# Optimization experiments

Measured on AMD Instinct MI355X. Metric: run time of the kernel, lower is better.

Reference implementation:

```python
import jax, jax.numpy as jnp
import numpy as np

NU = 8192   # num_users
NI = 8192   # num_items
B = 4096    # batch_size
D = 64      # embed_size
NS = 5      # num_scores


def _w(key, fan_in, fan_out):
    # xavier-uniform-like init
    lim = np.sqrt(6.0 / (fan_in + fan_out)).astype(np.float32)
    return jax.random.uniform(key, (fan_in, fan_out), jnp.float32, -lim, lim)


def setup_inputs() -> dict:
    key = jax.random.key(0)
    ks = jax.random.split(key, 32)
    z = lambda n: jnp.zeros((n,), jnp.float32)
    inp = {
        "batch_user": jax.random.randint(ks[0], (B,), 0, NU),
        "batch_item": jax.random.randint(ks[1], (B,), 0, NI),
        "R": jax.random.uniform(ks[2], (NU, NI), jnp.float32),
        "S": jax.random.uniform(ks[3], (NU, NU), jnp.float32),
        "U": _w(ks[4], NU, D),
        "V": _w(ks[5], NI, D),
        "w_r": _w(ks[6], NS, D), "b_r": z(D),
        "Wu0": _w(ks[7], 2 * D, D), "bu0": z(D), "Wu1": _w(ks[8], D, D), "bu1": z(D),
        "Wv0": _w(ks[9], 2 * D, D), "bv0": z(D), "Wv1": _w(ks[10], D, D), "bv1": z(D),
        "Wc0": _w(ks[11], 2 * D, D), "bc0": z(D), "Wc1": _w(ks[12], D, D), "bc1": z(D),
        "Wg0": _w(ks[13], 2 * D, D), "bg0": z(D), "Wg1": _w(ks[14], D, D), "bg1": z(D),
        "W_I": _w(ks[15], D, D), "b_I": z(D),
        "W_Sm": _w(ks[16], D, D), "b_Sm": z(D),
        "W1A": _w(ks[17], 2 * D, D), "b1A": z(D), "w2A": _w(ks[18], D, 1), "b2A": z(1),
        "W1B": _w(ks[19], 2 * D, D), "b1B": z(D), "w2B": _w(ks[20], D, 1), "b2B": z(1),
        "W1M": _w(ks[21], 2 * D, D), "b1M": z(D), "w2M": _w(ks[22], D, 1), "b2M": z(1),
        "W_Z": _w(ks[23], D, D), "b_Z": z(D),
    }
    return inp


def reference(batch_user, batch_item, R, S, U, V, w_r, b_r,
              Wu0, bu0, Wu1, bu1, Wv0, bv0, Wv1, bv1,
              Wc0, bc0, Wc1, bc1, Wg0, bg0, Wg1, bg1,
              W_I, b_I, W_Sm, b_Sm,
              W1A, b1A, w2A, b2A, W1B, b1B, w2B, b2B,
              W1M, b1M, w2M, b2M, W_Z, b_Z):
    relu = jax.nn.relu
    # rating embedding: e_r = Linear(num_scores->d) applied to vector [1..num_scores]
    e_r = jnp.arange(1, w_r.shape[0] + 1, dtype=w_r.dtype) @ w_r + b_r  # [d]
    Uc = jnp.concatenate([U, jnp.broadcast_to(e_r, U.shape)], axis=1)  # [NU, 2d]
    Vc = jnp.concatenate([V, jnp.broadcast_to(e_r, V.shape)], axis=1)  # [NI, 2d]
    # per-node MLP stacks (num_layer=2; layer0: 2d->d, layer1: d->d)
    Uh = relu(relu(Uc @ Wu0 + bu0) @ Wu1 + bu1)  # [NU, d]
    Vh = relu(relu(Vc @ Wv0 + bv0) @ Wv1 + bv1)  # [NI, d]
    Ub = Uh[batch_user]  # [B, d]
    Vb = Vh[batch_item]  # [B, d]
    # item-space attention A over batch, softmax along batch dim
    A = jax.nn.softmax(relu(jnp.concatenate([Vb, Ub], axis=1) @ W1A + b1A) @ w2A + b2A, axis=0)  # [B,1]
    # attention-weighted sparse-row aggregation over item embeddings
    H_I = relu(((R[batch_user] * A) @ Vh) @ W_I + b_I)  # [B, d]
    Bw = jax.nn.softmax(relu(jnp.concatenate([H_I, Ub], axis=1) @ W1B + b1B) @ w2B + b2B, axis=0)  # [B,1]
    H_S = relu(((S[batch_user] * Bw) @ Uh) @ W_Sm + b_Sm)  # [B, d]
    H = jnp.concatenate([H_I, H_S], axis=1)  # [B, 2d]
    H = relu(relu(H @ Wc0 + bc0) @ Wc1 + bc1)  # [B, d]
    M = jax.nn.softmax(relu(jnp.concatenate([Ub, Vb], axis=1) @ W1M + b1M) @ w2M + b2M, axis=0)  # [B,1]
    # R.T row-gather: columns of R for batch items -> [B, NU]
    Rt_b = jnp.take(R, batch_item, axis=1).T
    Z = relu(((Rt_b * M) @ Uh) @ W_Z + b_Z)  # [B, d]
    G = jnp.concatenate([H, Z], axis=1)  # [B, 2d]
    G = relu(relu(G @ Wg0 + bg0) @ Wg1 + bg1)  # [B, d]
    return G
```

## Files before the change

### kernel.cpp

```cpp
#include <hip/hip_runtime.h>
#include <stdint.h>


typedef short bf16x8 __attribute__((ext_vector_type(8)));
typedef float f32x4 __attribute__((ext_vector_type(4)));

__device__ __forceinline__ unsigned f2bf1(float f) {
    unsigned x = __float_as_uint(f);
    return (x + 0x7FFFu + ((x >> 16) & 1u)) >> 16;
}

__device__ __forceinline__ float wsum(float v) {
    #pragma unroll
    for (int o = 32; o; o >>= 1) v += __shfl_xor(v, o);
    return v;
}

__device__ __forceinline__ void block_softmax_stats(const float* __restrict__ s,
                                                    float& m, float& inv) {
    __shared__ float r1[4];
    __shared__ float r2[4];
    int t = threadIdx.x, lane = t & 63, wv = t >> 6;
    float lm = -3.4e38f;
    #pragma unroll
    for (int i = 0; i < 16; ++i) lm = fmaxf(lm, s[t + 256 * i]);
    #pragma unroll
    for (int o = 32; o; o >>= 1) lm = fmaxf(lm, __shfl_xor(lm, o));
    if (lane == 0) r1[wv] = lm;
    __syncthreads();
    m = fmaxf(fmaxf(r1[0], r1[1]), fmaxf(r1[2], r1[3]));
    float ls = 0.f;
    #pragma unroll
    for (int i = 0; i < 16; ++i) ls += __expf(s[t + 256 * i] - m);
    ls = wsum(ls);
    if (lane == 0) r2[wv] = ls;
    __syncthreads();
    inv = 1.f / (r2[0] + r2[1] + r2[2] + r2[3]);
}

__global__ __launch_bounds__(256) void k_mlp(
    const float* __restrict__ U, const float* __restrict__ V,
    const float* __restrict__ w_r, const float* __restrict__ b_r,
    const float* __restrict__ Wu0, const float* __restrict__ bu0,
    const float* __restrict__ Wu1, const float* __restrict__ bu1,
    const float* __restrict__ Wv0, const float* __restrict__ bv0,
    const float* __restrict__ Wv1, const float* __restrict__ bv1,
    float* __restrict__ Uh, float* __restrict__ Vh,
    unsigned short* __restrict__ Uhb, unsigned short* __restrict__ Vhb)
{
    int gt = blockIdx.x * 256 + threadIdx.x;
    int wid = gt >> 6;
    int lane = gt & 63;

    float er = b_r[lane];
    #pragma unroll
    for (int s = 0; s < 5; ++s) er += (float)(s + 1) * w_r[s * 64 + lane];

    const int isV = (wid >= 2048);
    const float* X  = isV ? V   : U;
    const float* W0 = isV ? Wv0 : Wu0;
    const float* B0 = isV ? bv0 : bu0;
    const float* W1 = isV ? Wv1 : Wu1;
    const float* B1 = isV ? bv1 : bu1;
    float* Hout          = isV ? Vh  : Uh;
    unsigned short* Hb   = isV ? Vhb : Uhb;
    int r0 = (wid & 2047) * 4;

    float x[4];
    #pragma unroll
    for (int j = 0; j < 4; ++j) x[j] = X[(r0 + j) * 64 + lane];

    float h0c = B0[lane];
    for (int k = 0; k < 64; ++k) h0c += __shfl(er, k) * W0[(64 + k) * 64 + lane];

    float h0[4];
    #pragma unroll
    for (int j = 0; j < 4; ++j) h0[j] = h0c;
    for (int k = 0; k < 64; ++k) {
        float wv = W0[k * 64 + lane];
        #pragma unroll
        for (int j = 0; j < 4; ++j) h0[j] += __shfl(x[j], k) * wv;
    }
    #pragma unroll
    for (int j = 0; j < 4; ++j) h0[j] = fmaxf(h0[j], 0.f);

    float h1[4];
    #pragma unroll
    for (int j = 0; j < 4; ++j) h1[j] = B1[lane];
    for (int k = 0; k < 64; ++k) {
        float wv = W1[k * 64 + lane];
        #pragma unroll
        for (int j = 0; j < 4; ++j) h1[j] += __shfl(h0[j], k) * wv;
    }
    #pragma unroll
    for (int j = 0; j < 4; ++j) {
        h1[j] = fmaxf(h1[j], 0.f);
        Hout[(r0 + j) * 64 + lane] = h1[j];
    }
    unsigned pw[2];
    #pragma unroll
    for (int q = 0; q < 2; ++q) pw[q] = f2bf1(h1[2*q]) | (f2bf1(h1[2*q+1]) << 16);
    unsigned short* dst = Hb + (size_t)(r0 >> 3) * 512 + (lane >> 4) * 128
                        + (lane & 15) * 8 + (r0 & 7);
    *(uint2*)dst = make_uint2(pw[0], pw[1]);
}

__global__ __launch_bounds__(256, 8) void k_gemm(
    const float* __restrict__ R, const float* __restrict__ S,
    const int* __restrict__ bu,
    const unsigned short* __restrict__ Uhb, const unsigned short* __restrict__ Vhb,
    float* __restrict__ PpI, float* __restrict__ PpS, float* __restrict__ Qp,
    int nkz, int klen)
{
    int bid = blockIdx.x;
    int tid = threadIdx.x;
    int w = tid >> 6;
    int l = tid & 63;
    int lg = l >> 4, lr = l & 15;
    int kiters = klen >> 5;
    int gP = nkz << 6;

    f32x4 acc[4] = {};

    if (bid < 2 * gP) {
        const int isS = bid >= gP;
        int q = isS ? bid - gP : bid;
        int tile = q & 63, kz = q >> 6;
        int brow = tile * 64 + w * 16 + lr;
        int ridx = bu[brow];
        const float* A = (isS ? S : R) + (size_t)ridx * 8192 + kz * klen + lg * 8;
        const unsigned short* Bb = (isS ? Uhb : Vhb)
                                 + (size_t)((kz * klen) >> 3) * 512 + lr * 8;
        f32x4 c0 = ((const f32x4*)A)[0];
        f32x4 c1 = ((const f32x4*)A)[1];
        #pragma unroll 2
        for (int ks = 0; ks < kiters; ++ks) {
            int nxt = (ks + 1 < kiters) ? ks + 1 : ks;
            f32x4 n0 = ((const f32x4*)(A + nxt * 32))[0];
            f32x4 n1 = ((const f32x4*)(A + nxt * 32))[1];
            union { bf16x8 v; unsigned u[4]; } af;
            af.u[0] = f2bf1(c0.x) | (f2bf1(c0.y) << 16);
            af.u[1] = f2bf1(c0.z) | (f2bf1(c0.w) << 16);
            af.u[2] = f2bf1(c1.x) | (f2bf1(c1.y) << 16);
            af.u[3] = f2bf1(c1.z) | (f2bf1(c1.w) << 16);
            const unsigned short* bp = Bb + (size_t)(ks * 4 + lg) * 512;
            #pragma unroll
            for (int c = 0; c < 4; ++c) {
                bf16x8 bf = *(const bf16x8*)(bp + c * 128);
                acc[c] = __builtin_amdgcn_mfma_f32_16x16x32_bf16(af.v, bf, acc[c], 0, 0, 0);
            }
            c0 = n0; c1 = n1;
        }
        float* out = (isS ? PpS : PpI)
                   + (size_t)(kz * 4096 + tile * 64 + w * 16 + lg * 4) * 64 + lr;
        #pragma unroll
        for (int c = 0; c < 4; ++c) {
            #pragma unroll
            for (int j = 0; j < 4; ++j) out[j * 64 + c * 16] = acc[c][j];
        }
    } else {
        int q = bid - 2 * gP;
        int tile = q & 127, kz = q >> 7;
        int icol = tile * 64 + w * 16 + lr;
        const float* A = R + (size_t)(kz * klen + lg * 8) * 8192 + icol;
        const unsigned short* Bb = Uhb + (size_t)((kz * klen) >> 3) * 512 + lr * 8;
        float cv[8];
        #pragma unroll
        for (int j = 0; j < 8; ++j) cv[j] = A[(size_t)j * 8192];
        #pragma unroll 2
        for (int ks = 0; ks < kiters; ++ks) {
            int nxt = (ks + 1 < kiters) ? ks + 1 : ks;
            const float* np = A + (size_t)nxt * 32 * 8192;
            float nv[8];
            #pragma unroll
            for (int j = 0; j < 8; ++j) nv[j] = np[(size_t)j * 8192];
            union { bf16x8 v; unsigned u[4]; } af;
            #pragma unroll
            for (int qq = 0; qq < 4; ++qq)
                af.u[qq] = f2bf1(cv[2*qq]) | (f2bf1(cv[2*qq+1]) << 16);
            const unsigned short* bp = Bb + (size_t)(ks * 4 + lg) * 512;
            #pragma unroll
            for (int c = 0; c < 4; ++c) {
                bf16x8 bf = *(const bf16x8*)(bp + c * 128);
                acc[c] = __builtin_amdgcn_mfma_f32_16x16x32_bf16(af.v, bf, acc[c], 0, 0, 0);
            }
            #pragma unroll
            for (int j = 0; j < 8; ++j) cv[j] = nv[j];
        }
        float* out = Qp + (size_t)(kz * 8192 + tile * 64 + w * 16 + lg * 4) * 64 + lr;
        #pragma unroll
        for (int c = 0; c < 4; ++c) {
            #pragma unroll
            for (int j = 0; j < 4; ++j) out[j * 64 + c * 16] = acc[c][j];
        }
    }
}

__global__ __launch_bounds__(256) void k_scoreAM(
    const int* __restrict__ bu, const int* __restrict__ bi,
    const float* __restrict__ Uh, const float* __restrict__ Vh,
    const float* __restrict__ W1A, const float* __restrict__ b1A,
    const float* __restrict__ w2A, const float* __restrict__ b2A,
    const float* __restrict__ W1M, const float* __restrict__ b1M,
    const float* __restrict__ w2M, const float* __restrict__ b2M,
    float* __restrict__ sA, float* __restrict__ sM)
{
    int gt = blockIdx.x * 256 + threadIdx.x;
    int wid = gt >> 6, lane = gt & 63;
    int b0 = wid * 2;
    float ub[2], vb[2];
    #pragma unroll
    for (int j = 0; j < 2; ++j) {
        ub[j] = Uh[(size_t)bu[b0 + j] * 64 + lane];
        vb[j] = Vh[(size_t)bi[b0 + j] * 64 + lane];
    }
    float hA[2], hM[2];
    #pragma unroll
    for (int j = 0; j < 2; ++j) { hA[j] = b1A[lane]; hM[j] = b1M[lane]; }
    for (int k = 0; k < 64; ++k) {
        float wa0 = W1A[k * 64 + lane], wa1 = W1A[(64 + k) * 64 + lane];
        float wm0 = W1M[k * 64 + lane], wm1 = W1M[(64 + k) * 64 + lane];
        #pragma unroll
        for (int j = 0; j < 2; ++j) {
            float sv = __shfl(vb[j], k), su = __shfl(ub[j], k);
            hA[j] += sv * wa0 + su * wa1;
            hM[j] += su * wm0 + sv * wm1;
        }
    }
    float w2a = w2A[lane], w2m = w2M[lane];
    #pragma unroll
    for (int j = 0; j < 2; ++j) {
        float sa = wsum(fmaxf(hA[j], 0.f) * w2a);
        float sm = wsum(fmaxf(hM[j], 0.f) * w2m);
        if (lane == 0) { sA[b0 + j] = sa + b2A[0]; sM[b0 + j] = sm + b2M[0]; }
    }
}

__global__ __launch_bounds__(256) void k_HI_scoreB(
    const float* __restrict__ PpI, const float* __restrict__ sA,
    const int* __restrict__ bu, const float* __restrict__ Uh,
    const float* __restrict__ W_I, const float* __restrict__ b_I,
    const float* __restrict__ W1B, const float* __restrict__ b1B,
    const float* __restrict__ w2B, const float* __restrict__ b2B,
    float* __restrict__ HI, float* __restrict__ sB, int nkz)
{
    float m, inv;
    block_softmax_stats(sA, m, inv);
    int wid = blockIdx.x * 4 + (threadIdx.x >> 6);
    int lane = threadIdx.x & 63;
    int b0 = wid * 2;
    float p[2];
    #pragma unroll
    for (int j = 0; j < 2; ++j) {
        int b = b0 + j;
        float a = 0.f;
        for (int kz = 0; kz < nkz; ++kz)
            a += PpI[(size_t)(kz * 4096 + b) * 64 + lane];
        p[j] = a * (__expf(sA[b] - m) * inv);
    }
    float h[2];
    #pragma unroll
    for (int j = 0; j < 2; ++j) h[j] = b_I[lane];
    for (int k = 0; k < 64; ++k) {
        float wv = W_I[k * 64 + lane];
        #pragma unroll
        for (int j = 0; j < 2; ++j) h[j] += __shfl(p[j], k) * wv;
    }
    float ub[2];
    #pragma unroll
    for (int j = 0; j < 2; ++j) {
        h[j] = fmaxf(h[j], 0.f);
        HI[(size_t)(b0 + j) * 64 + lane] = h[j];
        ub[j] = Uh[(size_t)bu[b0 + j] * 64 + lane];
    }
    float h2[2];
    #pragma unroll
    for (int j = 0; j < 2; ++j) h2[j] = b1B[lane];
    for (int k = 0; k < 64; ++k) {
        float w0 = W1B[k * 64 + lane], w1 = W1B[(64 + k) * 64 + lane];
        #pragma unroll
        for (int j = 0; j < 2; ++j) h2[j] += __shfl(h[j], k) * w0 + __shfl(ub[j], k) * w1;
    }
    float w2 = w2B[lane];
    #pragma unroll
    for (int j = 0; j < 2; ++j) {
        float sv = wsum(fmaxf(h2[j], 0.f) * w2);
        if (lane == 0) sB[b0 + j] = sv + b2B[0];
    }
}

__global__ __launch_bounds__(256) void k_HS_H(
    const float* __restrict__ PpS, const float* __restrict__ sB,
    const float* __restrict__ HI,
    const float* __restrict__ W_Sm, const float* __restrict__ b_Sm,
    const float* __restrict__ Wc0, const float* __restrict__ bc0,
    const float* __restrict__ Wc1, const float* __restrict__ bc1,
    float* __restrict__ Hout, int nkz)
{
    float m, inv;
    block_softmax_stats(sB, m, inv);
    int wid = blockIdx.x * 4 + (threadIdx.x >> 6);
    int lane = threadIdx.x & 63;
    int b0 = wid * 2;
    float p[2];
    #pragma unroll
    for (int j = 0; j < 2; ++j) {
        int b = b0 + j;
        float a = 0.f;
        for (int kz = 0; kz < nkz; ++kz)
            a += PpS[(size_t)(kz * 4096 + b) * 64 + lane];
        p[j] = a * (__expf(sB[b] - m) * inv);
    }
    float hs[2];
    #pragma unroll
    for (int j = 0; j < 2; ++j) hs[j] = b_Sm[lane];
    for (int k = 0; k < 64; ++k) {
        float wv = W_Sm[k * 64 + lane];
        #pragma unroll
        for (int j = 0; j < 2; ++j) hs[j] += __shfl(p[j], k) * wv;
    }
    float hi[2];
    #pragma unroll
    for (int j = 0; j < 2; ++j) {
        hs[j] = fmaxf(hs[j], 0.f);
        hi[j] = HI[(size_t)(b0 + j) * 64 + lane];
    }
    float h0[2];
    #pragma unroll
    for (int j = 0; j < 2; ++j) h0[j] = bc0[lane];
    for (int k = 0; k < 64; ++k) {
        float w0 = Wc0[k * 64 + lane], w1 = Wc0[(64 + k) * 64 + lane];
        #pragma unroll
        for (int j = 0; j < 2; ++j) h0[j] += __shfl(hi[j], k) * w0 + __shfl(hs[j], k) * w1;
    }
    #pragma unroll
    for (int j = 0; j < 2; ++j) h0[j] = fmaxf(h0[j], 0.f);
    float h1[2];
    #pragma unroll
    for (int j = 0; j < 2; ++j) h1[j] = bc1[lane];
    for (int k = 0; k < 64; ++k) {
        float wv = Wc1[k * 64 + lane];
        #pragma unroll
        for (int j = 0; j < 2; ++j) h1[j] += __shfl(h0[j], k) * wv;
    }
    #pragma unroll
    for (int j = 0; j < 2; ++j) Hout[(size_t)(b0 + j) * 64 + lane] = fmaxf(h1[j], 0.f);
}

__global__ __launch_bounds__(256) void k_Z_G(
    const float* __restrict__ Qp, const float* __restrict__ sM,
    const int* __restrict__ bi, const float* __restrict__ H,
    const float* __restrict__ W_Z, const float* __restrict__ b_Z,
    const float* __restrict__ Wg0, const float* __restrict__ bg0,
    const float* __restrict__ Wg1, const float* __restrict__ bg1,
    float* __restrict__ G, int nkz)
{
    float m, inv;
    block_softmax_stats(sM, m, inv);
    int wid = blockIdx.x * 4 + (threadIdx.x >> 6);
    int lane = threadIdx.x & 63;
    int b0 = wid * 2;
    float p[2];
    #pragma unroll
    for (int j = 0; j < 2; ++j) {
        int b = b0 + j;
        int it = bi[b];
        float a = 0.f;
        for (int kz = 0; kz < nkz; ++kz)
            a += Qp[(size_t)(kz * 8192 + it) * 64 + lane];
        p[j] = a * (__expf(sM[b] - m) * inv);
    }
    float z[2];
    #pragma unroll
    for (int j = 0; j < 2; ++j) z[j] = b_Z[lane];
    for (int k = 0; k < 64; ++k) {
        float wv = W_Z[k * 64 + lane];
        #pragma unroll
        for (int j = 0; j < 2; ++j) z[j] += __shfl(p[j], k) * wv;
    }
    float hr[2];
    #pragma unroll
    for (int j = 0; j < 2; ++j) {
        z[j] = fmaxf(z[j], 0.f);
        hr[j] = H[(size_t)(b0 + j) * 64 + lane];
    }
    float g0[2];
    #pragma unroll
    for (int j = 0; j < 2; ++j) g0[j] = bg0[lane];
    for (int k = 0; k < 64; ++k) {
        float w0 = Wg0[k * 64 + lane], w1 = Wg0[(64 + k) * 64 + lane];
        #pragma unroll
        for (int j = 0; j < 2; ++j) g0[j] += __shfl(hr[j], k) * w0 + __shfl(z[j], k) * w1;
    }
    #pragma unroll
    for (int j = 0; j < 2; ++j) g0[j] = fmaxf(g0[j], 0.f);
    float g1[2];
    #pragma unroll
    for (int j = 0; j < 2; ++j) g1[j] = bg1[lane];
    for (int k = 0; k < 64; ++k) {
        float wv = Wg1[k * 64 + lane];
        #pragma unroll
        for (int j = 0; j < 2; ++j) g1[j] += __shfl(g0[j], k) * wv;
    }
    #pragma unroll
    for (int j = 0; j < 2; ++j) G[(size_t)(b0 + j) * 64 + lane] = fmaxf(g1[j], 0.f);
}

extern "C" void kernel_launch(void* const* d_in, const int* in_sizes, int n_in,
                              void* d_out, int out_size, void* d_ws, size_t ws_size,
                              hipStream_t stream)
{
    (void)in_sizes; (void)n_in; (void)out_size;
    const int*   bu  = (const int*)  d_in[0];
    const int*   bi  = (const int*)  d_in[1];
    const float* R   = (const float*)d_in[2];
    const float* S   = (const float*)d_in[3];
    const float* U   = (const float*)d_in[4];
    const float* V   = (const float*)d_in[5];
    const float* w_r = (const float*)d_in[6];
    const float* b_r = (const float*)d_in[7];
    const float* Wu0 = (const float*)d_in[8];
    const float* bu0 = (const float*)d_in[9];
    const float* Wu1 = (const float*)d_in[10];
    const float* bu1 = (const float*)d_in[11];
    const float* Wv0 = (const float*)d_in[12];
    const float* bv0 = (const float*)d_in[13];
    const float* Wv1 = (const float*)d_in[14];
    const float* bv1 = (const float*)d_in[15];
    const float* Wc0 = (const float*)d_in[16];
    const float* bc0 = (const float*)d_in[17];
    const float* Wc1 = (const float*)d_in[18];
    const float* bc1 = (const float*)d_in[19];
    const float* Wg0 = (const float*)d_in[20];
    const float* bg0 = (const float*)d_in[21];
    const float* Wg1 = (const float*)d_in[22];
    const float* bg1 = (const float*)d_in[23];
    const float* W_I = (const float*)d_in[24];
    const float* b_I = (const float*)d_in[25];
    const float* W_Sm= (const float*)d_in[26];
    const float* b_Sm= (const float*)d_in[27];
    const float* W1A = (const float*)d_in[28];
    const float* b1A = (const float*)d_in[29];
    const float* w2A = (const float*)d_in[30];
    const float* b2A = (const float*)d_in[31];
    const float* W1B = (const float*)d_in[32];
    const float* b1B = (const float*)d_in[33];
    const float* w2B = (const float*)d_in[34];
    const float* b2B = (const float*)d_in[35];
    const float* W1M = (const float*)d_in[36];
    const float* b1M = (const float*)d_in[37];
    const float* w2M = (const float*)d_in[38];
    const float* b2M = (const float*)d_in[39];
    const float* W_Z = (const float*)d_in[40];
    const float* b_Z = (const float*)d_in[41];

    const int nkz  = (ws_size >= (42ull << 20)) ? 8 : 4;
    const int klen = 8192 / nkz;

    char* ws = (char*)d_ws;
    size_t off = 0;
    float*          Uh  = (float*)(ws + off);          off += 2ull << 20;
    float*          Vh  = (float*)(ws + off);          off += 2ull << 20;
    unsigned short* Uhb = (unsigned short*)(ws + off); off += 1ull << 20;
    unsigned short* Vhb = (unsigned short*)(ws + off); off += 1ull << 20;
    float*          PpI = (float*)(ws + off);          off += (size_t)nkz << 20;
    float*          PpS = (float*)(ws + off);          off += (size_t)nkz << 20;
    float*          Qp  = (float*)(ws + off);          off += (size_t)(2 * nkz) << 20;
    float*          sA  = (float*)(ws + off);
    float*          sM  = sA + 4096;
    float*          sB  = sA + 8192;                   off += 3 * 4096 * 4 + 4096;
    float*          HI  = (float*)(ws + off);          off += 1ull << 20;
    float*          Hh  = (float*)(ws + off);

    k_mlp<<<1024, 256, 0, stream>>>(U, V, w_r, b_r, Wu0, bu0, Wu1, bu1,
                                    Wv0, bv0, Wv1, bv1, Uh, Vh, Uhb, Vhb);
    int gP = nkz * 64, gQ = nkz * 128;
    k_gemm<<<2 * gP + gQ, 256, 0, stream>>>(R, S, bu, Uhb, Vhb, PpI, PpS, Qp,
                                            nkz, klen);
    k_scoreAM<<<512, 256, 0, stream>>>(bu, bi, Uh, Vh, W1A, b1A, w2A, b2A,
                                       W1M, b1M, w2M, b2M, sA, sM);
    k_HI_scoreB<<<512, 256, 0, stream>>>(PpI, sA, bu, Uh, W_I, b_I,
                                         W1B, b1B, w2B, b2B, HI, sB, nkz);
    k_HS_H<<<512, 256, 0, stream>>>(PpS, sB, HI, W_Sm, b_Sm, Wc0, bc0, Wc1, bc1,
                                    Hh, nkz);
    k_Z_G<<<512, 256, 0, stream>>>(Qp, sM, bi, Hh, W_Z, b_Z, Wg0, bg0, Wg1, bg1,
                                   (float*)d_out, nkz);
}
```

Before: 241.5 us.

## Split GEMM into Q and P kernels with LDS-staged R loads and deeper prefetch

Splits the combined GEMM kernel into two kernels. The R-transpose product (Qp) now stages 32x64 tiles of R through double-buffered LDS using global_load_lds, so global reads are coalesced 16-byte rows instead of strided per-column scalar loads. The gathered-row product (Pp) gets a 4-deep register prefetch ring in place of the previous 1-deep one. NKZ is fixed at compile time at 8 instead of being chosen from the workspace size, which adds a dependency on having enough workspace and an extra kernel launch.

```diff
diff --git a/kernel.cpp b/kernel.cpp
--- a/kernel.cpp
+++ b/kernel.cpp
@@ -4,6 +4,10 @@
 
 typedef short bf16x8 __attribute__((ext_vector_type(8)));
 typedef float f32x4 __attribute__((ext_vector_type(4)));
+
+#define NKZ    8
+#define KLEN   1024
+#define KITERS 32
 
 __device__ __forceinline__ unsigned f2bf1(float f) {
     unsigned x = __float_as_uint(f);
@@ -105,94 +109,139 @@
     *(uint2*)dst = make_uint2(pw[0], pw[1]);
 }
 
-__global__ __launch_bounds__(256, 8) void k_gemm(
+__global__ __launch_bounds__(256) void k_gemmQ(
+    const float* __restrict__ R,
+    const unsigned short* __restrict__ Uhb,
+    float* __restrict__ Qp)
+{
+    __shared__ float lds[2][2048];
+    const int tile = blockIdx.x & 127;
+    const int kz   = blockIdx.x >> 7;
+    const int i0 = tile * 64;
+    const int u0 = kz * KLEN;
+    const int t = threadIdx.x;
+    const int w = t >> 6, l = t & 63, lg = l >> 4, lr = l & 15;
+
+    f32x4 acc[4] = {};
+
+    const float* gbase = R + ((size_t)u0 + (t >> 4)) * 8192 + i0 + (t & 15) * 4;
+
+    #pragma unroll
+    for (int q = 0; q < 2; ++q) {
+        const float* g = gbase + (size_t)(q * 16) * 8192;
+        __builtin_amdgcn_global_load_lds(
+            (const __attribute__((address_space(1))) void*)g,
+            (__attribute__((address_space(3))) void*)&lds[0][(q * 256 + t) * 4],
+            16, 0, 0);
+    }
+    __syncthreads();
+
+    const int iloc = w * 16 + lr;
+    for (int s = 0; s < KITERS; ++s) {
+        if (s + 1 < KITERS) {
+            int nb = (s + 1) & 1;
+            #pragma unroll
+            for (int q = 0; q < 2; ++q) {
+                const float* g = gbase + (size_t)((s + 1) * 32 + q * 16) * 8192;
+                __builtin_amdgcn_global_load_lds(
+                    (const __attribute__((address_space(1))) void*)g,
+                    (__attribute__((address_space(3))) void*)&lds[nb][(q * 256 + t) * 4],
+                    16, 0, 0);
+            }
+        }
+        const float* Lb = lds[s & 1];
+        float av[8];
+        #pragma unroll
+        for (int j = 0; j < 8; ++j) av[j] = Lb[(8 * lg + j) * 64 + iloc];
+        union { bf16x8 v; unsigned u[4]; } af;
+        #pragma unroll
+        for (int q = 0; q < 4; ++q)
+            af.u[q] = f2bf1(av[2*q]) | (f2bf1(av[2*q+1]) << 16);
+        const unsigned short* bp = Uhb + (size_t)((u0 >> 3) + s * 4 + lg) * 512 + lr * 8;
+        #pragma unroll
+        for (int c = 0; c < 4; ++c) {
+            bf16x8 bf = *(const bf16x8*)(bp + c * 128);
+            acc[c] = __builtin_amdgcn_mfma_f32_16x16x32_bf16(af.v, bf, acc[c], 0, 0, 0);
+        }
+        __syncthreads();
+    }
+
+    float* out = Qp + (size_t)(kz * 8192 + tile * 64 + w * 16 + lg * 4) * 64 + lr;
+    #pragma unroll
+    for (int c = 0; c < 4; ++c) {
+        #pragma unroll
+        for (int j = 0; j < 4; ++j) out[j * 64 + c * 16] = acc[c][j];
+    }
+}
+
+__global__ __launch_bounds__(256) void k_gemmP(
     const float* __restrict__ R, const float* __restrict__ S,
     const int* __restrict__ bu,
     const unsigned short* __restrict__ Uhb, const unsigned short* __restrict__ Vhb,
-    float* __restrict__ PpI, float* __restrict__ PpS, float* __restrict__ Qp,
-    int nkz, int klen)
-{
+    float* __restrict__ PpI, float* __restrict__ PpS)
+{
+    const int gP = NKZ * 64;
     int bid = blockIdx.x;
+    const int isS = bid >= gP;
+    int q = isS ? bid - gP : bid;
+    int tile = q & 63, kz = q >> 6;
     int tid = threadIdx.x;
-    int w = tid >> 6;
-    int l = tid & 63;
+    int w = tid >> 6, l = tid & 63;
     int lg = l >> 4, lr = l & 15;
-    int kiters = klen >> 5;
-    int gP = nkz << 6;
+
+    int brow = tile * 64 + w * 16 + lr;
+    int ridx = bu[brow];
+    const float* A = (isS ? S : R) + (size_t)ridx * 8192 + kz * KLEN + lg * 8;
+    const unsigned short* Bb = (isS ? Uhb : Vhb)
+                             + (size_t)((kz * KLEN) >> 3) * 512 + lr * 8;
 
     f32x4 acc[4] = {};
-
-    if (bid < 2 * gP) {
-        const int isS = bid >= gP;
-        int q = isS ? bid - gP : bid;
-        int tile = q & 63, kz = q >> 6;
-        int brow = tile * 64 + w * 16 + lr;
-        int ridx = bu[brow];
-        const float* A = (isS ? S : R) + (size_t)ridx * 8192 + kz * klen + lg * 8;
-        const unsigned short* Bb = (isS ? Uhb : Vhb)
-                                 + (size_t)((kz * klen) >> 3) * 512 + lr * 8;
-        f32x4 c0 = ((const f32x4*)A)[0];
-        f32x4 c1 = ((const f32x4*)A)[1];
-        #pragma unroll 2
-        for (int ks = 0; ks < kiters; ++ks) {
-            int nxt = (ks + 1 < kiters) ? ks + 1 : ks;
-            f32x4 n0 = ((const f32x4*)(A + nxt * 32))[0];
-            f32x4 n1 = ((const f32x4*)(A + nxt * 32))[1];
-            union { bf16x8 v; unsigned u[4]; } af;
-            af.u[0] = f2bf1(c0.x) | (f2bf1(c0.y) << 16);
-            af.u[1] = f2bf1(c0.z) | (f2bf1(c0.w) << 16);
-            af.u[2] = f2bf1(c1.x) | (f2bf1(c1.y) << 16);
-            af.u[3] = f2bf1(c1.z) | (f2bf1(c1.w) << 16);
-            const unsigned short* bp = Bb + (size_t)(ks * 4 + lg) * 512;
-            #pragma unroll
-            for (int c = 0; c < 4; ++c) {
-                bf16x8 bf = *(const bf16x8*)(bp + c * 128);
-                acc[c] = __builtin_amdgcn_mfma_f32_16x16x32_bf16(af.v, bf, acc[c], 0, 0, 0);
-            }
-            c0 = n0; c1 = n1;
+    f32x4 b0[4], b1[4];
+    #pragma unroll
+    for (int d = 0; d < 4; ++d) {
+        b0[d] = ((const f32x4*)(A + d * 32))[0];
+        b1[d] = ((const f32x4*)(A + d * 32))[1];
+    }
+
+    #pragma unroll 4
+    for (int ks = 0; ks < KITERS - 4; ++ks) {
+        const int slot = ks & 3;
+        union { bf16x8 v; unsigned u[4]; } af;
+        af.u[0] = f2bf1(b0[slot].x) | (f2bf1(b0[slot].y) << 16);
+        af.u[1] = f2bf1(b0[slot].z) | (f2bf1(b0[slot].w) << 16);
+        af.u[2] = f2bf1(b1[slot].x) | (f2bf1(b1[slot].y) << 16);
+        af.u[3] = f2bf1(b1[slot].z) | (f2bf1(b1[slot].w) << 16);
+        b0[slot] = ((const f32x4*)(A + (ks + 4) * 32))[0];
+        b1[slot] = ((const f32x4*)(A + (ks + 4) * 32))[1];
+        const unsigned short* bp = Bb + (size_t)(ks * 4 + lg) * 512;
+        #pragma unroll
+        for (int c = 0; c < 4; ++c) {
+            bf16x8 bf = *(const bf16x8*)(bp + c * 128);
+            acc[c] = __builtin_amdgcn_mfma_f32_16x16x32_bf16(af.v, bf, acc[c], 0, 0, 0);
         }
-        float* out = (isS ? PpS : PpI)
-                   + (size_t)(kz * 4096 + tile * 64 + w * 16 + lg * 4) * 64 + lr;
+    }
+    #pragma unroll
+    for (int ks = KITERS - 4; ks < KITERS; ++ks) {
+        const int slot = ks & 3;
+        union { bf16x8 v; unsigned u[4]; } af;
+        af.u[0] = f2bf1(b0[slot].x) | (f2bf1(b0[slot].y) << 16);
+        af.u[1] = f2bf1(b0[slot].z) | (f2bf1(b0[slot].w) << 16);
+        af.u[2] = f2bf1(b1[slot].x) | (f2bf1(b1[slot].y) << 16);
+        af.u[3] = f2bf1(b1[slot].z) | (f2bf1(b1[slot].w) << 16);
+        const unsigned short* bp = Bb + (size_t)(ks * 4 + lg) * 512;
         #pragma unroll
         for (int c = 0; c < 4; ++c) {
-            #pragma unroll
-            for (int j = 0; j < 4; ++j) out[j * 64 + c * 16] = acc[c][j];
+            bf16x8 bf = *(const bf16x8*)(bp + c * 128);
+            acc[c] = __builtin_amdgcn_mfma_f32_16x16x32_bf16(af.v, bf, acc[c], 0, 0, 0);
         }
-    } else {
-        int q = bid - 2 * gP;
-        int tile = q & 127, kz = q >> 7;
-        int icol = tile * 64 + w * 16 + lr;
-        const float* A = R + (size_t)(kz * klen + lg * 8) * 8192 + icol;
-        const unsigned short* Bb = Uhb + (size_t)((kz * klen) >> 3) * 512 + lr * 8;
-        float cv[8];
-        #pragma unroll
-        for (int j = 0; j < 8; ++j) cv[j] = A[(size_t)j * 8192];
-        #pragma unroll 2
-        for (int ks = 0; ks < kiters; ++ks) {
-            int nxt = (ks + 1 < kiters) ? ks + 1 : ks;
-            const float* np = A + (size_t)nxt * 32 * 8192;
-            float nv[8];
-            #pragma unroll
-            for (int j = 0; j < 8; ++j) nv[j] = np[(size_t)j * 8192];
-            union { bf16x8 v; unsigned u[4]; } af;
-            #pragma unroll
-            for (int qq = 0; qq < 4; ++qq)
-                af.u[qq] = f2bf1(cv[2*qq]) | (f2bf1(cv[2*qq+1]) << 16);
-            const unsigned short* bp = Bb + (size_t)(ks * 4 + lg) * 512;
-            #pragma unroll
-            for (int c = 0; c < 4; ++c) {
-                bf16x8 bf = *(const bf16x8*)(bp + c * 128);
-                acc[c] = __builtin_amdgcn_mfma_f32_16x16x32_bf16(af.v, bf, acc[c], 0, 0, 0);
-            }
-            #pragma unroll
-            for (int j = 0; j < 8; ++j) cv[j] = nv[j];
-        }
-        float* out = Qp + (size_t)(kz * 8192 + tile * 64 + w * 16 + lg * 4) * 64 + lr;
-        #pragma unroll
-        for (int c = 0; c < 4; ++c) {
-            #pragma unroll
-            for (int j = 0; j < 4; ++j) out[j * 64 + c * 16] = acc[c][j];
-        }
+    }
+
+    float* out = (isS ? PpS : PpI)
+               + (size_t)(kz * 4096 + tile * 64 + w * 16 + lg * 4) * 64 + lr;
+    #pragma unroll
+    for (int c = 0; c < 4; ++c) {
+        #pragma unroll
+        for (int j = 0; j < 4; ++j) out[j * 64 + c * 16] = acc[c][j];
     }
 }
 
@@ -242,7 +291,7 @@
     const float* __restrict__ W_I, const float* __restrict__ b_I,
     const float* __restrict__ W1B, const float* __restrict__ b1B,
     const float* __restrict__ w2B, const float* __restrict__ b2B,
-    float* __restrict__ HI, float* __restrict__ sB, int nkz)
+    float* __restrict__ HI, float* __restrict__ sB)
 {
     float m, inv;
     block_softmax_stats(sA, m, inv);
@@ -254,7 +303,8 @@
     for (int j = 0; j < 2; ++j) {
         int b = b0 + j;
         float a = 0.f;
-        for (int kz = 0; kz < nkz; ++kz)
+        #pragma unroll
+        for (int kz = 0; kz < NKZ; ++kz)
             a += PpI[(size_t)(kz * 4096 + b) * 64 + lane];
         p[j] = a * (__expf(sA[b] - m) * inv);
     }
@@ -295,7 +345,7 @@
     const float* __restrict__ W_Sm, const float* __restrict__ b_Sm,
     const float* __restrict__ Wc0, const float* __restrict__ bc0,
     const float* __restrict__ Wc1, const float* __restrict__ bc1,
-    float* __restrict__ Hout, int nkz)
+    float* __restrict__ Hout)
 {
     float m, inv;
     block_softmax_stats(sB, m, inv);
@@ -307,7 +357,8 @@
     for (int j = 0; j < 2; ++j) {
         int b = b0 + j;
         float a = 0.f;
-        for (int kz = 0; kz < nkz; ++kz)
+        #pragma unroll
+        for (int kz = 0; kz < NKZ; ++kz)
             a += PpS[(size_t)(kz * 4096 + b) * 64 + lane];
         p[j] = a * (__expf(sB[b] - m) * inv);
     }
@@ -353,7 +404,7 @@
     const float* __restrict__ W_Z, const float* __restrict__ b_Z,
     const float* __restrict__ Wg0, const float* __restrict__ bg0,
     const float* __restrict__ Wg1, const float* __restrict__ bg1,
-    float* __restrict__ G, int nkz)
+    float* __restrict__ G)
 {
     float m, inv;
     block_softmax_stats(sM, m, inv);
@@ -366,7 +417,8 @@
         int b = b0 + j;
         int it = bi[b];
         float a = 0.f;
-        for (int kz = 0; kz < nkz; ++kz)
+        #pragma unroll
+        for (int kz = 0; kz < NKZ; ++kz)
             a += Qp[(size_t)(kz * 8192 + it) * 64 + lane];
         p[j] = a * (__expf(sM[b] - m) * inv);
     }
@@ -410,7 +462,7 @@
                               void* d_out, int out_size, void* d_ws, size_t ws_size,
                               hipStream_t stream)
 {
-    (void)in_sizes; (void)n_in; (void)out_size;
+    (void)in_sizes; (void)n_in; (void)out_size; (void)ws_size;
     const int*   bu  = (const int*)  d_in[0];
     const int*   bi  = (const int*)  d_in[1];
     const float* R   = (const float*)d_in[2];
@@ -454,18 +506,15 @@
     const float* W_Z = (const float*)d_in[40];
     const float* b_Z = (const float*)d_in[41];
 
-    const int nkz  = (ws_size >= (42ull << 20)) ? 8 : 4;
-    const int klen = 8192 / nkz;
-
     char* ws = (char*)d_ws;
     size_t off = 0;
     float*          Uh  = (float*)(ws + off);          off += 2ull << 20;
     float*          Vh  = (float*)(ws + off);          off += 2ull << 20;
     unsigned short* Uhb = (unsigned short*)(ws + off); off += 1ull << 20;
     unsigned short* Vhb = (unsigned short*)(ws + off); off += 1ull << 20;
-    float*          PpI = (float*)(ws + off);          off += (size_t)nkz << 20;
-    float*          PpS = (float*)(ws + off);          off += (size_t)nkz << 20;
-    float*          Qp  = (float*)(ws + off);          off += (size_t)(2 * nkz) << 20;
+    float*          PpI = (float*)(ws + off);          off += (size_t)NKZ << 20;
+    float*          PpS = (float*)(ws + off);          off += (size_t)NKZ << 20;
+    float*          Qp  = (float*)(ws + off);          off += (size_t)(2 * NKZ) << 20;
     float*          sA  = (float*)(ws + off);
     float*          sM  = sA + 4096;
     float*          sB  = sA + 8192;                   off += 3 * 4096 * 4 + 4096;
@@ -474,15 +523,14 @@
 
     k_mlp<<<1024, 256, 0, stream>>>(U, V, w_r, b_r, Wu0, bu0, Wu1, bu1,
                                     Wv0, bv0, Wv1, bv1, Uh, Vh, Uhb, Vhb);
-    int gP = nkz * 64, gQ = nkz * 128;
-    k_gemm<<<2 * gP + gQ, 256, 0, stream>>>(R, S, bu, Uhb, Vhb, PpI, PpS, Qp,
-                                            nkz, klen);
+    k_gemmQ<<<128 * NKZ, 256, 0, stream>>>(R, Uhb, Qp);
+    k_gemmP<<<2 * NKZ * 64, 256, 0, stream>>>(R, S, bu, Uhb, Vhb, PpI, PpS);
     k_scoreAM<<<512, 256, 0, stream>>>(bu, bi, Uh, Vh, W1A, b1A, w2A, b2A,
                                        W1M, b1M, w2M, b2M, sA, sM);
     k_HI_scoreB<<<512, 256, 0, stream>>>(PpI, sA, bu, Uh, W_I, b_I,
-                                         W1B, b1B, w2B, b2B, HI, sB, nkz);
+                                         W1B, b1B, w2B, b2B, HI, sB);
     k_HS_H<<<512, 256, 0, stream>>>(PpS, sB, HI, W_Sm, b_Sm, Wc0, bc0, Wc1, bc1,
-                                    Hh, nkz);
+                                    Hh);
     k_Z_G<<<512, 256, 0, stream>>>(Qp, sM, bi, Hh, W_Z, b_Z, Wg0, bg0, Wg1, bg1,
-                                   (float*)d_out, nkz);
-}
+                                   (float*)d_out);
+}
```

Result: faster. 224.1 us (-7.2%).
